# Kernel tuning notes

Measured on AMD Instinct MI355X. Metric: run time of the kernel, lower is better.

## Reference

```python
import jax, jax.numpy as jnp
import numpy as np

B = 2048      # batchsize from init_kwargs
TAU = 0.5     # temperature from init_kwargs
EPS = 1e-8    # torch CosineSimilarity eps


def _neg_idx(b):
    # For each row i of the (2B,2B) similarity matrix, the columns that are
    # negatives: everything except the diagonal (i) and the positive partner
    # ((i+B) mod 2B). Matches torch mask 1-(eye(k=B)+eye(k=-B)+eye()).
    n = 2 * b
    rows = np.arange(n)
    partner = (rows + b) % n
    cols = np.tile(np.arange(n), (n, 1))
    mask = (cols != rows[:, None]) & (cols != partner[:, None])
    return cols[mask].reshape(n, n - 2)


NEG_IDX = jnp.asarray(_neg_idx(B))  # (2B, 2B-2), int


def setup_inputs() -> dict:
    key = jax.random.key(0)
    k1, k2 = jax.random.split(key)
    D = 1024
    return {
        "z_orig": jax.random.normal(k1, (B, D), dtype=jnp.float32),
        "z_augment": jax.random.normal(k2, (B, D), dtype=jnp.float32),
    }


def reference(z_orig, z_augment):
    n = 2 * B
    z = jnp.concatenate([z_augment, z_orig], axis=0)            # (2B, D)
    norms = jnp.linalg.norm(z, axis=-1, keepdims=True)
    zn = z / jnp.maximum(norms, EPS)
    sim = zn @ zn.T                                             # (2B, 2B) cosine sims
    idx = jnp.arange(n)
    pos = sim[idx, (idx + B) % n]                               # (2B,) positive pairs
    neg = jnp.take_along_axis(sim, NEG_IDX, axis=1)             # (2B, 2B-2)
    logits = jnp.concatenate([pos[:, None], neg], axis=1) / TAU # (2B, 2B-1)
    # CrossEntropy with label 0, reduction='sum':
    loss = jnp.sum(jax.nn.logsumexp(logits, axis=1) - logits[:, 0])
    return loss / n
```

## Files before the change

### kernel.cpp

```cpp
#include <hip/hip_runtime.h>
#include <hip/hip_bf16.h>
#include <math.h>


#define BB   2048
#define N2   4096
#define DIM  1024
#define TAUI 2.0f
#define EPSN 1e-8f

#define BM  128
#define BN  128
#define BKK 64
#define NP  ((N2 / BN) * 2)

typedef __attribute__((ext_vector_type(4))) float f32x4;
typedef __attribute__((ext_vector_type(8))) short s16x8;

__device__ __forceinline__ void gll16(const void* g, void* l) {
    __builtin_amdgcn_global_load_lds(
        (const __attribute__((address_space(1))) void*)g,
        (__attribute__((address_space(3))) void*)l, 16, 0, 0);
}

__global__ __launch_bounds__(256) void k_prep(const float* __restrict__ zO,
                                              const float* __restrict__ zA,
                                              __hip_bfloat16* __restrict__ zb) {
    int row = blockIdx.x;
    const float* zr = (row < BB) ? (zA + (size_t)row * DIM)
                                 : (zO + (size_t)(row - BB) * DIM);
    int t = threadIdx.x;
    float4 v = *(const float4*)(zr + t * 4);
    float s = v.x * v.x + v.y * v.y + v.z * v.z + v.w * v.w;
    for (int m = 1; m < 64; m <<= 1) s += __shfl_xor(s, m);
    __shared__ float wsum[4];
    __shared__ float inv_s;
    int wv = t >> 6, ln = t & 63;
    if (ln == 0) wsum[wv] = s;
    __syncthreads();
    if (t == 0)
        inv_s = 1.0f / fmaxf(sqrtf(wsum[0] + wsum[1] + wsum[2] + wsum[3]), EPSN);
    __syncthreads();
    float inv = inv_s;
    __hip_bfloat16 h0 = __float2bfloat16(v.x * inv);
    __hip_bfloat16 h1 = __float2bfloat16(v.y * inv);
    __hip_bfloat16 h2 = __float2bfloat16(v.z * inv);
    __hip_bfloat16 h3 = __float2bfloat16(v.w * inv);
    ushort4 o;
    o.x = *(unsigned short*)&h0;
    o.y = *(unsigned short*)&h1;
    o.z = *(unsigned short*)&h2;
    o.w = *(unsigned short*)&h3;
    ((ushort4*)zb)[(size_t)row * (DIM / 4) + t] = o;
}

__global__ __launch_bounds__(256) void k_lse(const __hip_bfloat16* __restrict__ zb,
                                             float* __restrict__ pm,
                                             float* __restrict__ pl,
                                             float* __restrict__ pos) {
    __shared__ __hip_bfloat16 As[BM * BKK];
    __shared__ __hip_bfloat16 Bs[BN * BKK];

    int itile = blockIdx.x, jtile = blockIdx.y;
    int ibase = itile * BM, jbase = jtile * BN;
    int tid = threadIdx.x;
    int w = tid >> 6, l = tid & 63;
    int wr = w >> 1, wc = w & 1;
    int rl = l & 15, kg = l >> 4;

    const __hip_bfloat16* Ag = zb + (size_t)ibase * DIM;
    const __hip_bfloat16* Bg = zb + (size_t)jbase * DIM;

    f32x4 acc[4][4];
#pragma unroll
    for (int m = 0; m < 4; m++)
#pragma unroll
        for (int n = 0; n < 4; n++) acc[m][n] = (f32x4){0.f, 0.f, 0.f, 0.f};

    int srow = l >> 3;
    int scol = (l & 7) * 8;

    for (int kt = 0; kt < DIM; kt += BKK) {
        __syncthreads();
#pragma unroll
        for (int s4 = 0; s4 < 4; s4++) {
            int s = w * 4 + s4;
            int grow = 8 * s + srow;
            gll16(Ag + (size_t)grow * DIM + kt + scol, &As[s * 512]);
            gll16(Bg + (size_t)grow * DIM + kt + scol, &Bs[s * 512]);
        }
        __syncthreads();

#pragma unroll
        for (int kk = 0; kk < 2; kk++) {
            s16x8 a[4], b[4];
#pragma unroll
            for (int m = 0; m < 4; m++)
                a[m] = *(const s16x8*)&As[(wr * 64 + m * 16 + rl) * BKK + kk * 32 + kg * 8];
#pragma unroll
            for (int n = 0; n < 4; n++)
                b[n] = *(const s16x8*)&Bs[(wc * 64 + n * 16 + rl) * BKK + kk * 32 + kg * 8];
#pragma unroll
            for (int m = 0; m < 4; m++)
#pragma unroll
                for (int n = 0; n < 4; n++)
                    acc[m][n] = __builtin_amdgcn_mfma_f32_16x16x32_bf16(
                        a[m], b[n], acc[m][n], 0, 0, 0);
        }
    }

    int rowbase = ibase + wr * 64;
    int colbase = jbase + wc * 64;
    int slot = jtile * 2 + wc;
#pragma unroll
    for (int m = 0; m < 4; m++) {
#pragma unroll
        for (int r = 0; r < 4; r++) {
            int ig = rowbase + m * 16 + kg * 4 + r;
            int pp = (ig + BB) & (N2 - 1);
            float v[4];
            float rmax = -1e30f;
#pragma unroll
            for (int n = 0; n < 4; n++) {
                int jg = colbase + n * 16 + rl;
                float val = acc[m][n][r] * TAUI;
                if (jg == pp) pos[ig] = val;
                if (jg == ig) val = -1e30f;
                v[n] = val;
                rmax = fmaxf(rmax, val);
            }
#pragma unroll
            for (int mk = 1; mk < 16; mk <<= 1)
                rmax = fmaxf(rmax, __shfl_xor(rmax, mk));
            float ssum = 0.f;
#pragma unroll
            for (int n = 0; n < 4; n++) ssum += __expf(v[n] - rmax);
#pragma unroll
            for (int mk = 1; mk < 16; mk <<= 1) ssum += __shfl_xor(ssum, mk);
            if (rl == 0) {
                pm[slot * N2 + ig] = rmax;
                pl[slot * N2 + ig] = ssum;
            }
        }
    }
}

__global__ __launch_bounds__(128) void k_combine(const float* __restrict__ pm,
                                                 const float* __restrict__ pl,
                                                 const float* __restrict__ pos,
                                                 float* __restrict__ out) {
    int row = blockIdx.x * 128 + threadIdx.x;
    float M = -1e30f;
#pragma unroll
    for (int c = 0; c < NP; c++) M = fmaxf(M, pm[c * N2 + row]);
    float S = 0.f;
#pragma unroll
    for (int c = 0; c < NP; c++) S += pl[c * N2 + row] * __expf(pm[c * N2 + row] - M);
    float v = M + __logf(S) - pos[row];
    for (int mk = 1; mk < 64; mk <<= 1) v += __shfl_xor(v, mk);
    __shared__ float w0;
    if (threadIdx.x == 0) w0 = v;
    __syncthreads();
    if (threadIdx.x == 64) atomicAdd(out, (v + w0) * (1.0f / (float)N2));
}

extern "C" void kernel_launch(void* const* d_in, const int* in_sizes, int n_in,
                              void* d_out, int out_size, void* d_ws, size_t ws_size,
                              hipStream_t stream) {
    const float* zO = (const float*)d_in[0];
    const float* zA = (const float*)d_in[1];
    float* out = (float*)d_out;

    __hip_bfloat16* zb = (__hip_bfloat16*)d_ws;
    float* pm  = (float*)((char*)d_ws + (size_t)N2 * DIM * 2);
    float* pl  = pm + NP * N2;
    float* pos = pl + NP * N2;

    hipMemsetAsync(out, 0, sizeof(float), stream);
    k_prep<<<N2, 256, 0, stream>>>(zO, zA, zb);
    k_lse<<<dim3(N2 / BM, N2 / BN), 256, 0, stream>>>(zb, pm, pl, pos);
    k_combine<<<N2 / 128, 128, 0, stream>>>(pm, pl, pos, out);
}
```

Measured before the change: 147.5 us.

## Exploit symmetry of similarity matrix by computing only upper-triangular tiles

Since the similarity matrix is symmetric, the LSE kernel now launches only the 528 upper-triangular 128x128 tiles instead of all 1024. Off-diagonal tiles also produce column-wise partial max/sum statistics for the transposed block. The partial buffers are switched to a row-major layout so the combine kernel reads contiguous slots per row. This roughly halves GEMM work at the cost of extra epilogue reductions, strided partial writes, and a sqrt-based tile index decode.

```diff
diff --git a/kernel.cpp b/kernel.cpp
--- a/kernel.cpp
+++ b/kernel.cpp
@@ -12,7 +12,8 @@
 #define BM  128
 #define BN  128
 #define BKK 64
-#define NP  ((N2 / BN) * 2)
+#define NP  64
+#define NBLK 528
 
 typedef __attribute__((ext_vector_type(4))) float f32x4;
 typedef __attribute__((ext_vector_type(8))) short s16x8;
@@ -61,8 +62,13 @@
     __shared__ __hip_bfloat16 As[BM * BKK];
     __shared__ __hip_bfloat16 Bs[BN * BKK];
 
-    int itile = blockIdx.x, jtile = blockIdx.y;
-    int ibase = itile * BM, jbase = jtile * BN;
+    int lin = blockIdx.x;
+    int ti = (int)((65.0f - sqrtf(4225.0f - 8.0f * (float)lin)) * 0.5f);
+    while ((ti + 1) * (65 - (ti + 1)) / 2 <= lin) ti++;
+    while (ti * (65 - ti) / 2 > lin) ti--;
+    int tj = ti + (lin - ti * (65 - ti) / 2);
+
+    int ibase = ti * BM, jbase = tj * BN;
     int tid = threadIdx.x;
     int w = tid >> 6, l = tid & 63;
     int wr = w >> 1, wc = w & 1;
@@ -111,7 +117,7 @@
 
     int rowbase = ibase + wr * 64;
     int colbase = jbase + wc * 64;
-    int slot = jtile * 2 + wc;
+    int slot = tj * 2 + wc;
 #pragma unroll
     for (int m = 0; m < 4; m++) {
 #pragma unroll
@@ -124,7 +130,7 @@
             for (int n = 0; n < 4; n++) {
                 int jg = colbase + n * 16 + rl;
                 float val = acc[m][n][r] * TAUI;
-                if (jg == pp) pos[ig] = val;
+                if (jg == pp) { pos[ig] = val; pos[jg] = val; }
                 if (jg == ig) val = -1e30f;
                 v[n] = val;
                 rmax = fmaxf(rmax, val);
@@ -138,30 +144,62 @@
 #pragma unroll
             for (int mk = 1; mk < 16; mk <<= 1) ssum += __shfl_xor(ssum, mk);
             if (rl == 0) {
-                pm[slot * N2 + ig] = rmax;
-                pl[slot * N2 + ig] = ssum;
+                pm[(size_t)ig * NP + slot] = rmax;
+                pl[(size_t)ig * NP + slot] = ssum;
             }
         }
     }
-}
-
-__global__ __launch_bounds__(128) void k_combine(const float* __restrict__ pm,
+
+    if (ti != tj) {
+        int slot2 = ti * 2 + wr;
+#pragma unroll
+        for (int n = 0; n < 4; n++) {
+            float cmax = -1e30f;
+#pragma unroll
+            for (int m = 0; m < 4; m++)
+#pragma unroll
+                for (int r = 0; r < 4; r++)
+                    cmax = fmaxf(cmax, acc[m][n][r] * TAUI);
+            cmax = fmaxf(cmax, __shfl_xor(cmax, 16));
+            cmax = fmaxf(cmax, __shfl_xor(cmax, 32));
+            float cs = 0.f;
+#pragma unroll
+            for (int m = 0; m < 4; m++)
+#pragma unroll
+                for (int r = 0; r < 4; r++)
+                    cs += __expf(acc[m][n][r] * TAUI - cmax);
+            cs += __shfl_xor(cs, 16);
+            cs += __shfl_xor(cs, 32);
+            if (l < 16) {
+                int jg = colbase + n * 16 + rl;
+                pm[(size_t)jg * NP + slot2] = cmax;
+                pl[(size_t)jg * NP + slot2] = cs;
+            }
+        }
+    }
+}
+
+__global__ __launch_bounds__(256) void k_combine(const float* __restrict__ pm,
                                                  const float* __restrict__ pl,
                                                  const float* __restrict__ pos,
                                                  float* __restrict__ out) {
-    int row = blockIdx.x * 128 + threadIdx.x;
+    int row = blockIdx.x * 256 + threadIdx.x;
+    const float* P = pm + (size_t)row * NP;
+    const float* L = pl + (size_t)row * NP;
     float M = -1e30f;
 #pragma unroll
-    for (int c = 0; c < NP; c++) M = fmaxf(M, pm[c * N2 + row]);
+    for (int c = 0; c < NP; c++) M = fmaxf(M, P[c]);
     float S = 0.f;
 #pragma unroll
-    for (int c = 0; c < NP; c++) S += pl[c * N2 + row] * __expf(pm[c * N2 + row] - M);
+    for (int c = 0; c < NP; c++) S += L[c] * __expf(P[c] - M);
     float v = M + __logf(S) - pos[row];
     for (int mk = 1; mk < 64; mk <<= 1) v += __shfl_xor(v, mk);
-    __shared__ float w0;
-    if (threadIdx.x == 0) w0 = v;
+    __shared__ float wsum[4];
+    int wv = threadIdx.x >> 6, ln = threadIdx.x & 63;
+    if (ln == 0) wsum[wv] = v;
     __syncthreads();
-    if (threadIdx.x == 64) atomicAdd(out, (v + w0) * (1.0f / (float)N2));
+    if (threadIdx.x == 0)
+        atomicAdd(out, (wsum[0] + wsum[1] + wsum[2] + wsum[3]) * (1.0f / (float)N2));
 }
 
 extern "C" void kernel_launch(void* const* d_in, const int* in_sizes, int n_in,
@@ -173,11 +211,11 @@
 
     __hip_bfloat16* zb = (__hip_bfloat16*)d_ws;
     float* pm  = (float*)((char*)d_ws + (size_t)N2 * DIM * 2);
-    float* pl  = pm + NP * N2;
-    float* pos = pl + NP * N2;
+    float* pl  = pm + (size_t)N2 * NP;
+    float* pos = pl + (size_t)N2 * NP;
 
     hipMemsetAsync(out, 0, sizeof(float), stream);
     k_prep<<<N2, 256, 0, stream>>>(zO, zA, zb);
-    k_lse<<<dim3(N2 / BM, N2 / BN), 256, 0, stream>>>(zb, pm, pl, pos);
-    k_combine<<<N2 / 128, 128, 0, stream>>>(pm, pl, pos, out);
-}
+    k_lse<<<NBLK, 256, 0, stream>>>(zb, pm, pl, pos);
+    k_combine<<<N2 / 256, 256, 0, stream>>>(pm, pl, pos, out);
+}
```

Result: faster. 133.8 us (-9.3%).
